# Optimization experiments

Hardware: AMD Instinct MI355X
Metric: run time of the kernel (lower is better)

Reference implementation:

```python
import jax, jax.numpy as jnp
import numpy as np

N, E = 50000, 800000
DIM_IN, DIM_OUT, HEADS, HID = 1000, 32, 8, 8
NEG_SLOPE = 0.2


def glorot(key, shape, fan_in, fan_out):
    s = jnp.sqrt(6.0 / (fan_in + fan_out))
    return jax.random.uniform(key, shape, jnp.float32, -s, s)


def setup_inputs() -> dict:
    key = jax.random.key(0)
    ks = jax.random.split(key, 16)
    x = jax.random.normal(ks[0], (N, DIM_IN), jnp.float32)
    edge_index = jax.random.randint(ks[1], (2, E), 0, N, jnp.int32)
    d2 = DIM_IN + HEADS * HID  # 1064
    p = {
        "x": x, "edge_index": edge_index,
        "W1": glorot(ks[2], (DIM_IN, HEADS * HID), DIM_IN, HEADS * HID),
        "as1": glorot(ks[3], (HEADS, HID), HID, HID),
        "ad1": glorot(ks[4], (HEADS, HID), HID, HID),
        "b1": jnp.zeros((HEADS * HID,), jnp.float32),
        "W2": glorot(ks[5], (d2, HEADS * HID), d2, HEADS * HID),
        "as2": glorot(ks[6], (HEADS, HID), HID, HID),
        "ad2": glorot(ks[7], (HEADS, HID), HID, HID),
        "b2": jnp.zeros((HEADS * HID,), jnp.float32),
        "W3": glorot(ks[8], (HEADS * HID, HEADS * DIM_OUT), HEADS * HID, HEADS * DIM_OUT),
        "as3": glorot(ks[9], (HEADS, DIM_OUT), DIM_OUT, DIM_OUT),
        "ad3": glorot(ks[10], (HEADS, DIM_OUT), DIM_OUT, DIM_OUT),
        "b3": jnp.zeros((DIM_OUT,), jnp.float32),
    }
    return p


def gat_conv(x, src, dst, W, a_src, a_dst, bias, heads, out_ch, concat):
    n = x.shape[0]
    h = (x @ W).reshape(n, heads, out_ch)           # [N,H,C]
    al_s = jnp.einsum("nhc,hc->nh", h, a_src)        # [N,H]
    al_d = jnp.einsum("nhc,hc->nh", h, a_dst)
    e = jax.nn.leaky_relu(al_s[src] + al_d[dst], NEG_SLOPE)  # [Etot,H]
    # segment softmax over incoming edges of each dst node
    m = jax.ops.segment_max(e, dst, num_segments=n)
    ee = jnp.exp(e - m[dst])
    denom = jax.ops.segment_sum(ee, dst, num_segments=n)
    alpha = ee / (denom[dst] + 1e-16)               # [Etot,H]
    msg = h[src] * alpha[..., None]                  # [Etot,H,C]
    out = jax.ops.segment_sum(msg, dst, num_segments=n)  # [N,H,C]
    out = out.reshape(n, heads * out_ch) if concat else out.mean(axis=1)
    return out + bias


def reference(x, edge_index, W1, as1, ad1, b1, W2, as2, ad2, b2, W3, as3, ad3, b3):
    n = x.shape[0]
    loops = jnp.arange(n, dtype=edge_index.dtype)
    src = jnp.concatenate([edge_index[0], loops])    # PyG adds self-loops
    dst = jnp.concatenate([edge_index[1], loops])
    h1 = jax.nn.elu(gat_conv(x, src, dst, W1, as1, ad1, b1, HEADS, HID, True))
    h2 = gat_conv(jnp.concatenate([x, h1], axis=1), src, dst, W2, as2, ad2, b2, HEADS, HID, True)
    h2 = jax.nn.elu(h2)
    h3 = gat_conv(h2, src, dst, W3, as3, ad3, b3, HEADS, DIM_OUT, False)
    return jax.nn.log_softmax(h3, axis=1)
```

## Files before the change

kernel.cpp:

```cpp
#include <hip/hip_runtime.h>
#include <hip/hip_bf16.h>

#define DIM_IN 1000
#define HEADS 8
#define HID 8
#define DIM_OUT 32
#define NEG_SLOPE 0.2f
#define EPAD 64

typedef __attribute__((ext_vector_type(4))) float f32x4;
typedef __attribute__((ext_vector_type(8))) short s16x8;

__device__ __forceinline__ unsigned bf16rne(float f) {
    unsigned u = __float_as_uint(f);
    return (u + 0x7FFFu + ((u >> 16) & 1u)) >> 16;
}
__device__ __forceinline__ unsigned pack2(float lo, float hi) {
    return bf16rne(lo) | (bf16rne(hi) << 16);
}
__device__ __forceinline__ float bflo(unsigned u) { return __uint_as_float(u << 16); }
__device__ __forceinline__ float bfhi(unsigned u) { return __uint_as_float(u & 0xFFFF0000u); }
__device__ __forceinline__ float bf1(ushort u) { return __uint_as_float((unsigned)u << 16); }

__global__ __launch_bounds__(256) void pack_all(
    const float* __restrict__ W1, const float* __restrict__ W2,
    const float* __restrict__ W3, const float* __restrict__ as3,
    const float* __restrict__ ad3, ushort* __restrict__ wpack,
    ushort* __restrict__ w3pack, float* __restrict__ wts,
    float* __restrict__ wtd)
{
    int b = blockIdx.x;
    if (b < 64) {
        int t = b * 256 + threadIdx.x;
        int lane = t & 63;
        int ctg = (t >> 6) & 7;
        int kt = t >> 9;
        int c = ctg * 16 + (lane & 15);
        int kbase = kt * 32 + (lane >> 4) * 8;
        ushort v[8] __attribute__((aligned(16)));
#pragma unroll
        for (int j = 0; j < 8; j++) {
            int k = kbase + j;
            float w = 0.f;
            if (k < DIM_IN) w = (c < 64) ? W1[(size_t)k * 64 + c] : W2[(size_t)k * 64 + (c - 64)];
            v[j] = (ushort)bf16rne(w);
        }
        *(uint4*)&wpack[(size_t)t * 8] = *(const uint4*)v;
    } else if (b < 72) {
        int t = (b - 64) * 256 + threadIdx.x;
        int lane = t & 63;
        int ctg = (t >> 6) & 15;
        int kt = t >> 10;
        int c = ctg * 16 + (lane & 15);
        int kbase = kt * 32 + (lane >> 4) * 8;
        ushort v[8] __attribute__((aligned(16)));
#pragma unroll
        for (int j = 0; j < 8; j++)
            v[j] = (ushort)bf16rne(W3[(size_t)(kbase + j) * 256 + c]);
        *(uint4*)&w3pack[(size_t)t * 8] = *(const uint4*)v;
    } else {
        int t = (b - 72) * 256 + threadIdx.x;
        if (t >= 512) return;
        int h = t >> 6, k = t & 63;
        float s = 0.f, d = 0.f;
#pragma unroll
        for (int c = 0; c < 32; c++) {
            float w = W3[(size_t)k * 256 + h * 32 + c];
            s += w * as3[h * 32 + c];
            d += w * ad3[h * 32 + c];
        }
        wts[h * 64 + k] = s;
        wtd[h * 64 + k] = d;
    }
}

__global__ __launch_bounds__(256) void zero_init(
    int* __restrict__ deg, int* __restrict__ esrc_pad, int N)
{
    int i = blockIdx.x * 256 + threadIdx.x;
    if (i < N) deg[i] = 0;
    if (i < EPAD) esrc_pad[i] = 0;
}

__global__ __launch_bounds__(256) void gemm1_mfma(
    const float* __restrict__ x, const ushort* __restrict__ wpack,
    ushort* __restrict__ hp1b, float* __restrict__ p2, int N)
{
    __shared__ __align__(16) ushort a_lds[2][32 * 32];
    const int tid = threadIdx.x;
    const int lane = tid & 63;
    const int wc = tid >> 6;
    const int rowbase = blockIdx.x * 32;

    const int srow = tid >> 3;
    const int skq = (tid & 7) * 4;
    const int sgr = rowbase + srow;
    const int sidx = ((srow >> 4) * 64 + (skq >> 3) * 16 + (srow & 15)) * 8 + (skq & 4);

    f32x4 acc[2][2];
#pragma unroll
    for (int i = 0; i < 2; i++)
#pragma unroll
        for (int j = 0; j < 2; j++) acc[i][j] = (f32x4){0.f, 0.f, 0.f, 0.f};

    float4 s0;
    auto load_stage = [&](int t) {
        int k0 = t * 32 + skq;
        s0 = make_float4(0.f, 0.f, 0.f, 0.f);
        if (sgr < N && k0 + 4 <= DIM_IN)
            s0 = *(const float4*)&x[(size_t)sgr * DIM_IN + k0];
    };
    auto store_stage = [&](int buf) {
        uint2 w;
        w.x = pack2(s0.x, s0.y);
        w.y = pack2(s0.z, s0.w);
        *(uint2*)&a_lds[buf][sidx] = w;
    };

    load_stage(0);
    store_stage(0);
    __syncthreads();

    const s16x8* wp = (const s16x8*)wpack;
    for (int t = 0; t < 32; t++) {
        int cur = t & 1;
        if (t + 1 < 32) load_stage(t + 1);
        s16x8 bf0 = wp[(size_t)(t * 8 + wc * 2 + 0) * 64 + lane];
        s16x8 bf1 = wp[(size_t)(t * 8 + wc * 2 + 1) * 64 + lane];
        s16x8 af0 = *(const s16x8*)&a_lds[cur][(0 * 64 + lane) * 8];
        s16x8 af1 = *(const s16x8*)&a_lds[cur][(1 * 64 + lane) * 8];
        acc[0][0] = __builtin_amdgcn_mfma_f32_16x16x32_bf16(af0, bf0, acc[0][0], 0, 0, 0);
        acc[0][1] = __builtin_amdgcn_mfma_f32_16x16x32_bf16(af0, bf1, acc[0][1], 0, 0, 0);
        acc[1][0] = __builtin_amdgcn_mfma_f32_16x16x32_bf16(af1, bf0, acc[1][0], 0, 0, 0);
        acc[1][1] = __builtin_amdgcn_mfma_f32_16x16x32_bf16(af1, bf1, acc[1][1], 0, 0, 0);
        if (t + 1 < 32) store_stage(cur ^ 1);
        __syncthreads();
    }

    const int colbase = wc * 32;
#pragma unroll
    for (int rt = 0; rt < 2; rt++) {
        int gr = rowbase + rt * 16 + ((lane >> 4) * 4);
#pragma unroll
        for (int ctl = 0; ctl < 2; ctl++) {
            int c = colbase + ctl * 16 + (lane & 15);
#pragma unroll
            for (int reg = 0; reg < 4; reg++) {
                int r = gr + reg;
                if (r >= N) continue;
                float v = acc[rt][ctl][reg];
                if (c < 64) hp1b[(size_t)r * 64 + c] = (ushort)bf16rne(v);
                else        p2[(size_t)r * 64 + (c - 64)] = v;
            }
        }
    }
}

__global__ __launch_bounds__(256) void gemm3_mfma(
    const ushort* __restrict__ h2b, const ushort* __restrict__ w3pack,
    ushort* __restrict__ h3pb, int N)
{
    const int tid = threadIdx.x;
    const int lane = tid & 63;
    const int wc = tid >> 6;
    const int rowbase = blockIdx.x * 16;
    const int arow = rowbase + (lane & 15);

    f32x4 acc[4];
#pragma unroll
    for (int i = 0; i < 4; i++) acc[i] = (f32x4){0.f, 0.f, 0.f, 0.f};

    const s16x8* wp = (const s16x8*)w3pack;
#pragma unroll
    for (int kt = 0; kt < 2; kt++) {
        s16x8 af = (s16x8){0, 0, 0, 0, 0, 0, 0, 0};
        if (arow < N)
            af = *(const s16x8*)&h2b[(size_t)arow * 64 + kt * 32 + (lane >> 4) * 8];
#pragma unroll
        for (int ct = 0; ct < 4; ct++) {
            s16x8 bf = wp[(size_t)(kt * 16 + wc * 4 + ct) * 64 + lane];
            acc[ct] = __builtin_amdgcn_mfma_f32_16x16x32_bf16(af, bf, acc[ct], 0, 0, 0);
        }
    }
#pragma unroll
    for (int ct = 0; ct < 4; ct++) {
        int col = wc * 64 + ct * 16 + (lane & 15);
        int gr = rowbase + (lane >> 4) * 4;
#pragma unroll
        for (int reg = 0; reg < 4; reg++) {
            int r = gr + reg;
            if (r < N) h3pb[(size_t)r * 256 + col] = (ushort)bf16rne(acc[ct][reg]);
        }
    }
}

__global__ __launch_bounds__(256) void gemm_k64_n64_acc(
    const float* __restrict__ A, const float* __restrict__ W,
    const float* __restrict__ P, ushort* __restrict__ outb, int N)
{
    __shared__ float as_[16][65];
    const int tid = threadIdx.x;
    const int rb = blockIdx.x * 16;
#pragma unroll
    for (int i = 0; i < 4; i++) {
        int idx = tid + i * 256;
        int r = idx >> 6, c = idx & 63;
        int gr = rb + r;
        as_[r][c] = (gr < N) ? A[(size_t)gr * 64 + c] : 0.f;
    }
    __syncthreads();
    const int row = tid >> 4;
    const int col = (tid & 15) * 4;
    float4 acc = {0, 0, 0, 0};
#pragma unroll 8
    for (int k = 0; k < 64; k++) {
        float a = as_[row][k];
        float4 w = *(const float4*)&W[k * 64 + col];
        acc.x += a * w.x; acc.y += a * w.y; acc.z += a * w.z; acc.w += a * w.w;
    }
    int gr = rb + row;
    if (gr < N) {
        float4 p = *(const float4*)&P[(size_t)gr * 64 + col];
        float v0 = p.x + acc.x, v1 = p.y + acc.y, v2 = p.z + acc.z, v3 = p.w + acc.w;
        *(uint*)&outb[(size_t)gr * 64 + col] = pack2(v0, v1);
        *(uint*)&outb[(size_t)gr * 64 + col + 2] = pack2(v2, v3);
    }
}

__global__ __launch_bounds__(256) void attn_dots_b8(
    const ushort* __restrict__ hb, const float* __restrict__ a_s,
    const float* __restrict__ a_d, float* __restrict__ als,
    float* __restrict__ ald, int NH)
{
    int i = blockIdx.x * blockDim.x + threadIdx.x;
    if (i >= NH) return;
    int head = i & 7;
    uint4 q = *(const uint4*)&hb[(size_t)i * 8];
    float f[8] = {bflo(q.x), bfhi(q.x), bflo(q.y), bfhi(q.y),
                  bflo(q.z), bfhi(q.z), bflo(q.w), bfhi(q.w)};
    const float* ap = a_s + head * 8;
    const float* dp = a_d + head * 8;
    float s = 0.f, d = 0.f;
#pragma unroll
    for (int c = 0; c < 8; c++) { s += f[c] * ap[c]; d += f[c] * dp[c]; }
    als[i] = s; ald[i] = d;
}

__global__ __launch_bounds__(256) void attn_dots_w(
    const ushort* __restrict__ h2b, const float* __restrict__ wts,
    const float* __restrict__ wtd, float* __restrict__ als,
    float* __restrict__ ald, int NH)
{
    int i = blockIdx.x * blockDim.x + threadIdx.x;
    if (i >= NH) return;
    int head = i & 7, node = i >> 3;
    const uint4* hp = (const uint4*)(h2b + (size_t)node * 64);
    const float* wsp = wts + head * 64;
    const float* wdp = wtd + head * 64;
    float s = 0.f, d = 0.f;
#pragma unroll
    for (int cq = 0; cq < 8; cq++) {
        uint4 q = hp[cq];
        float f0 = bflo(q.x), f1 = bfhi(q.x), f2 = bflo(q.y), f3 = bfhi(q.y);
        float f4 = bflo(q.z), f5 = bfhi(q.z), f6 = bflo(q.w), f7 = bfhi(q.w);
        int c = cq * 8;
        s += f0 * wsp[c] + f1 * wsp[c + 1] + f2 * wsp[c + 2] + f3 * wsp[c + 3]
           + f4 * wsp[c + 4] + f5 * wsp[c + 5] + f6 * wsp[c + 6] + f7 * wsp[c + 7];
        d += f0 * wdp[c] + f1 * wdp[c + 1] + f2 * wdp[c + 2] + f3 * wdp[c + 3]
           + f4 * wdp[c + 4] + f5 * wdp[c + 5] + f6 * wdp[c + 6] + f7 * wdp[c + 7];
    }
    als[i] = s; ald[i] = d;
}

__global__ __launch_bounds__(256) void csr_hist(
    const int* __restrict__ ei, int E, int Etot, int* __restrict__ deg)
{
    int e = blockIdx.x * blockDim.x + threadIdx.x;
    if (e >= Etot) return;
    int d = (e < E) ? ei[E + e] : e - E;
    atomicAdd(&deg[d], 1);
}

__global__ __launch_bounds__(256) void scan_partial(
    const int* __restrict__ deg, int* __restrict__ bsum, int N)
{
    __shared__ int red[256];
    int base = blockIdx.x * 1024;
    int t = threadIdx.x;
    int i0 = base + t * 4;
    int s = 0;
    if (i0 + 3 < N) {
        int4 v = *(const int4*)&deg[i0];
        s = v.x + v.y + v.z + v.w;
    } else {
#pragma unroll
        for (int j = 0; j < 4; j++) if (i0 + j < N) s += deg[i0 + j];
    }
    red[t] = s;
    __syncthreads();
    for (int off = 128; off; off >>= 1) {
        if (t < off) red[t] += red[t + off];
        __syncthreads();
    }
    if (t == 0) bsum[blockIdx.x] = red[0];
}

__global__ __launch_bounds__(64) void scan_bsums(
    const int* __restrict__ bsum, int* __restrict__ boff,
    int* __restrict__ rowptr, int nb, int N)
{
    __shared__ int sh[256];
    int t = threadIdx.x;
    for (int i = t; i < nb; i += 64) sh[i] = bsum[i];
    __syncthreads();
    if (t == 0) {
        int run = 0;
        for (int i = 0; i < nb; i++) { int x = sh[i]; sh[i] = run; run += x; }
        rowptr[N] = run;
    }
    __syncthreads();
    for (int i = t; i < nb; i += 64) boff[i] = sh[i];
}

__global__ __launch_bounds__(256) void scan_final(
    const int* __restrict__ deg, const int* __restrict__ boff,
    int* __restrict__ rowptr, int* __restrict__ cursor, int N)
{
    __shared__ int red[256];
    int base = blockIdx.x * 1024;
    int t = threadIdx.x;
    int i0 = base + t * 4;
    int v0 = 0, v1 = 0, v2 = 0, v3 = 0;
    if (i0 + 3 < N) {
        int4 v = *(const int4*)&deg[i0];
        v0 = v.x; v1 = v.y; v2 = v.z; v3 = v.w;
    } else {
        if (i0 < N) v0 = deg[i0];
        if (i0 + 1 < N) v1 = deg[i0 + 1];
        if (i0 + 2 < N) v2 = deg[i0 + 2];
        if (i0 + 3 < N) v3 = deg[i0 + 3];
    }
    red[t] = v0 + v1 + v2 + v3;
    __syncthreads();
    for (int off = 1; off < 256; off <<= 1) {
        int n = (t >= off) ? red[t - off] : 0;
        __syncthreads();
        red[t] += n;
        __syncthreads();
    }
    int excl = (t ? red[t - 1] : 0) + boff[blockIdx.x];
    if (i0 < N)     { rowptr[i0] = excl;     cursor[i0] = excl; }
    excl += v0;
    if (i0 + 1 < N) { rowptr[i0 + 1] = excl; cursor[i0 + 1] = excl; }
    excl += v1;
    if (i0 + 2 < N) { rowptr[i0 + 2] = excl; cursor[i0 + 2] = excl; }
    excl += v2;
    if (i0 + 3 < N) { rowptr[i0 + 3] = excl; cursor[i0 + 3] = excl; }
}

__global__ __launch_bounds__(256) void csr_fill(
    const int* __restrict__ ei, int E, int Etot,
    int* __restrict__ cursor, int* __restrict__ esrc)
{
    int e = blockIdx.x * blockDim.x + threadIdx.x;
    if (e >= Etot) return;
    int s, d;
    if (e < E) { s = ei[e]; d = ei[E + e]; } else { s = d = e - E; }
    int pos = atomicAdd(&cursor[d], 1);
    esrc[pos] = s;
}

template <bool OUT_BF16>
__global__ __launch_bounds__(256) void gat_gather64(
    const int* __restrict__ rowptr, const int* __restrict__ esrc,
    const float* __restrict__ als, const float* __restrict__ ald,
    const ushort* __restrict__ hb, const float* __restrict__ bias,
    float* __restrict__ outf, ushort* __restrict__ outb, int N)
{
    int node = blockIdx.x * 4 + (threadIdx.x >> 6);
    if (node >= N) return;
    int lane = threadIdx.x & 63;
    int head = lane >> 3;
    int start = rowptr[node];
    int cnt = rowptr[node + 1] - start;
    float aldv = ald[(size_t)node * 8 + head];
    const int* ip = esrc + start;

    float dA = 0.f, aA = 0.f;
    float dB = 0.f, aB = 0.f;

    auto idx4 = [&](int k) {
        int4 r; r.x = ip[k]; r.y = ip[k + 1]; r.z = ip[k + 2]; r.w = ip[k + 3];
        return r;
    };
    auto issue = [&](int4 s, float4& ee, float4& hh) {
        ee.x = als[(size_t)s.x * 8 + head];
        ee.y = als[(size_t)s.y * 8 + head];
        ee.z = als[(size_t)s.z * 8 + head];
        ee.w = als[(size_t)s.w * 8 + head];
        hh.x = bf1(hb[(size_t)s.x * 64 + lane]);
        hh.y = bf1(hb[(size_t)s.y * 64 + lane]);
        hh.z = bf1(hb[(size_t)s.z * 64 + lane]);
        hh.w = bf1(hb[(size_t)s.w * 64 + lane]);
    };
    auto lrelu = [&](float e, int k) {
        e += aldv;
        e = (e > 0.f) ? e : NEG_SLOPE * e;
        return (k < cnt) ? e : -1e30f;
    };
    auto upd = [&](int base, float4 ee, float4 hh) {
        if (base >= cnt) return;
        float x0 = __expf(lrelu(ee.x, base + 0));
        float x1 = __expf(lrelu(ee.y, base + 1));
        float x2 = __expf(lrelu(ee.z, base + 2));
        float x3 = __expf(lrelu(ee.w, base + 3));
        dA += x0; aA = fmaf(x0, hh.x, aA);
        dA += x1; aA = fmaf(x1, hh.y, aA);
        dB += x2; aB = fmaf(x2, hh.z, aB);
        dB += x3; aB = fmaf(x3, hh.w, aB);
    };

    int4 i0 = idx4(0), i1 = idx4(4);
    float4 e0, h0, e1, h1;
    issue(i0, e0, h0);
    int nb = (cnt + 3) >> 2;
    for (int b = 0; b < nb; b += 2) {
        i0 = idx4((b + 2) * 4);
        issue(i1, e1, h1);
        upd(b * 4, e0, h0);
        i1 = idx4((b + 3) * 4);
        issue(i0, e0, h0);
        upd((b + 1) * 4, e1, h1);
    }
    float den = dA + dB;
    float acc = aA + aB;
    float v = acc / (den + 1e-16f) + bias[lane];
    v = (v > 0.f) ? v : (__expf(v) - 1.f);
    if (OUT_BF16) outb[(size_t)node * 64 + lane] = (ushort)bf16rne(v);
    else outf[(size_t)node * 64 + lane] = v;
}

__global__ __launch_bounds__(256) void gat_l3_final(
    const int* __restrict__ rowptr, const int* __restrict__ esrc,
    const float* __restrict__ als, const float* __restrict__ ald,
    const ushort* __restrict__ h3pb, const float* __restrict__ b3,
    float* __restrict__ out, int N)
{
    int node = blockIdx.x * 4 + (threadIdx.x >> 6);
    if (node >= N) return;
    int lane = threadIdx.x & 63;
    int h = lane >> 3, c8 = lane & 7;
    int loff = h * 32 + c8 * 4;
    int start = rowptr[node];
    int cnt = rowptr[node + 1] - start;
    float aldv = ald[(size_t)node * 8 + h];
    const int* ip = esrc + start;

    float dA = 0.f, dB = 0.f;
    float4 accA = {0, 0, 0, 0}, accB = {0, 0, 0, 0};

    auto idx4 = [&](int k) {
        int4 r; r.x = ip[k]; r.y = ip[k + 1]; r.z = ip[k + 2]; r.w = ip[k + 3];
        return r;
    };
    auto issue = [&](int4 s, float4& ee, uint2& q0, uint2& q1, uint2& q2, uint2& q3) {
        ee.x = als[(size_t)s.x * 8 + h];
        ee.y = als[(size_t)s.y * 8 + h];
        ee.z = als[(size_t)s.z * 8 + h];
        ee.w = als[(size_t)s.w * 8 + h];
        q0 = *(const uint2*)&h3pb[(size_t)s.x * 256 + loff];
        q1 = *(const uint2*)&h3pb[(size_t)s.y * 256 + loff];
        q2 = *(const uint2*)&h3pb[(size_t)s.z * 256 + loff];
        q3 = *(const uint2*)&h3pb[(size_t)s.w * 256 + loff];
    };
    auto lrelu = [&](float e, int k) {
        e += aldv;
        e = (e > 0.f) ? e : NEG_SLOPE * e;
        return (k < cnt) ? e : -1e30f;
    };
    auto upedge = [&](float ee, uint2 q, float& d, float4& a) {
        d += ee;
        a.x = fmaf(ee, bflo(q.x), a.x);
        a.y = fmaf(ee, bfhi(q.x), a.y);
        a.z = fmaf(ee, bflo(q.y), a.z);
        a.w = fmaf(ee, bfhi(q.y), a.w);
    };
    auto upd = [&](int base, float4 ee, uint2 q0, uint2 q1, uint2 q2, uint2 q3) {
        if (base >= cnt) return;
        float x0 = __expf(lrelu(ee.x, base + 0));
        float x1 = __expf(lrelu(ee.y, base + 1));
        float x2 = __expf(lrelu(ee.z, base + 2));
        float x3 = __expf(lrelu(ee.w, base + 3));
        upedge(x0, q0, dA, accA);
        upedge(x1, q1, dA, accA);
        upedge(x2, q2, dB, accB);
        upedge(x3, q3, dB, accB);
    };

    int4 i0 = idx4(0), i1 = idx4(4);
    float4 eC, eD;
    uint2 q0C, q1C, q2C, q3C, q0D, q1D, q2D, q3D;
    issue(i0, eC, q0C, q1C, q2C, q3C);
    int nb = (cnt + 3) >> 2;
    for (int b = 0; b < nb; b += 2) {
        i0 = idx4((b + 2) * 4);
        issue(i1, eD, q0D, q1D, q2D, q3D);
        upd(b * 4, eC, q0C, q1C, q2C, q3C);
        i1 = idx4((b + 3) * 4);
        issue(i0, eC, q0C, q1C, q2C, q3C);
        upd((b + 1) * 4, eD, q0D, q1D, q2D, q3D);
    }

    float den = dA + dB;
    float inv = 1.f / (den + 1e-16f);
    float4 v;
    v.x = (accA.x + accB.x) * inv;
    v.y = (accA.y + accB.y) * inv;
    v.z = (accA.z + accB.z) * inv;
    v.w = (accA.w + accB.w) * inv;

#pragma unroll
    for (int o = 8; o < 64; o <<= 1) {
        v.x += __shfl_xor(v.x, o, 64);
        v.y += __shfl_xor(v.y, o, 64);
        v.z += __shfl_xor(v.z, o, 64);
        v.w += __shfl_xor(v.w, o, 64);
    }
    int cq = c8 * 4;
    v.x = v.x * 0.125f + b3[cq + 0];
    v.y = v.y * 0.125f + b3[cq + 1];
    v.z = v.z * 0.125f + b3[cq + 2];
    v.w = v.w * 0.125f + b3[cq + 3];
    float mx = fmaxf(fmaxf(v.x, v.y), fmaxf(v.z, v.w));
#pragma unroll
    for (int o = 1; o < 8; o <<= 1) mx = fmaxf(mx, __shfl_xor(mx, o, 64));
    float ex = __expf(v.x - mx) + __expf(v.y - mx) + __expf(v.z - mx) + __expf(v.w - mx);
#pragma unroll
    for (int o = 1; o < 8; o <<= 1) ex += __shfl_xor(ex, o, 64);
    float lse = mx + __logf(ex);
    if (lane < 8) {
        float4 r4 = {v.x - lse, v.y - lse, v.z - lse, v.w - lse};
        *(float4*)&out[(size_t)node * 32 + cq] = r4;
    }
}

extern "C" void kernel_launch(void* const* d_in, const int* in_sizes, int n_in,
                              void* d_out, int out_size, void* d_ws, size_t ws_size,
                              hipStream_t stream)
{
    const float* x   = (const float*)d_in[0];
    const int*   ei  = (const int*)  d_in[1];
    const float* W1  = (const float*)d_in[2];
    const float* as1 = (const float*)d_in[3];
    const float* ad1 = (const float*)d_in[4];
    const float* b1  = (const float*)d_in[5];
    const float* W2  = (const float*)d_in[6];
    const float* as2 = (const float*)d_in[7];
    const float* ad2 = (const float*)d_in[8];
    const float* b2  = (const float*)d_in[9];
    const float* W3  = (const float*)d_in[10];
    const float* as3 = (const float*)d_in[11];
    const float* ad3 = (const float*)d_in[12];
    const float* b3  = (const float*)d_in[13];
    float* out = (float*)d_out;

    const int N = in_sizes[0] / DIM_IN;
    const int E = in_sizes[1] / 2;
    const int Etot = E + N;

    float* ws = (float*)d_ws;
    size_t o = 0;
    float* p2  = ws + o; o += (size_t)N * 64;
    float* h1  = ws + o; o += (size_t)N * 64;
    ushort* hp1b  = (ushort*)(ws + o); o += (size_t)N * 32;
    ushort* h2pb  = (ushort*)(ws + o); o += (size_t)N * 32;
    ushort* h2b   = (ushort*)(ws + o); o += (size_t)N * 32;
    ushort* h3pb  = (ushort*)(ws + o); o += (size_t)N * 128;
    float* als = ws + o; o += (size_t)N * 8;
    float* ald = ws + o; o += (size_t)N * 8;
    float* wts = ws + o; o += 512;
    float* wtd = ws + o; o += 512;
    ushort* wpack  = (ushort*)(ws + o); o += 65536;
    ushort* w3pack = (ushort*)(ws + o); o += 8192;
    int* deg    = (int*)(ws + o); o += N;
    int* rowptr = (int*)(ws + o); o += N + 1;
    int* cursor = (int*)(ws + o); o += N;
    int* bsum   = (int*)(ws + o); o += 64;
    int* boff   = (int*)(ws + o); o += 64;
    int* esrc   = (int*)(ws + o); o += Etot + EPAD;
    if (o * 4 > ws_size) return;

    const int TB = 256;
    const int EG = (Etot + TB - 1) / TB;
    const int NB = (N + 1023) / 1024;

    pack_all<<<74, TB, 0, stream>>>(W1, W2, W3, as3, ad3, wpack, w3pack, wts, wtd);
    gemm1_mfma<<<(N + 31) / 32, TB, 0, stream>>>(x, wpack, hp1b, p2, N);

    zero_init<<<(N + TB - 1) / TB, TB, 0, stream>>>(deg, esrc + Etot, N);
    csr_hist<<<EG, TB, 0, stream>>>(ei, E, Etot, deg);
    scan_partial<<<NB, TB, 0, stream>>>(deg, bsum, N);
    scan_bsums<<<1, 64, 0, stream>>>(bsum, boff, rowptr, NB, N);
    scan_final<<<NB, TB, 0, stream>>>(deg, boff, rowptr, cursor, N);
    csr_fill<<<EG, TB, 0, stream>>>(ei, E, Etot, cursor, esrc);

    attn_dots_b8<<<(N * 8 + TB - 1) / TB, TB, 0, stream>>>(hp1b, as1, ad1, als, ald, N * 8);
    gat_gather64<false><<<(N + 3) / 4, TB, 0, stream>>>(rowptr, esrc, als, ald, hp1b, b1, h1, nullptr, N);

    gemm_k64_n64_acc<<<(N + 15) / 16, TB, 0, stream>>>(h1, W2 + (size_t)DIM_IN * 64, p2, h2pb, N);

    attn_dots_b8<<<(N * 8 + TB - 1) / TB, TB, 0, stream>>>(h2pb, as2, ad2, als, ald, N * 8);
    gat_gather64<true><<<(N + 3) / 4, TB, 0, stream>>>(rowptr, esrc, als, ald, h2pb, b2, nullptr, h2b, N);

    gemm3_mfma<<<(N + 15) / 16, TB, 0, stream>>>(h2b, w3pack, h3pb, N);
    attn_dots_w<<<(N * 8 + TB - 1) / TB, TB, 0, stream>>>(h2b, wts, wtd, als, ald, N * 8);
    gat_l3_final<<<(N + 3) / 4, TB, 0, stream>>>(rowptr, esrc, als, ald, h3pb, b3, out, N);
}
```

Baseline: 400.9 us.

## Sort nodes by degree for gather kernels and widen gemm1 loads to 8 floats

Adds a degree histogram, bin scan and counting-sort permutation so the three gather kernels process nodes grouped by in-degree. Nodes with similar edge counts then share a block, which is meant to reduce wave imbalance and tail latency. Separately, gemm1 now loads 8 floats per thread per stage and covers two K-steps per LDS buffer pair, which halves the number of barriers. The cost is three extra small kernels with atomics, an indirect perm lookup that makes output writes non-contiguous, and a larger LDS footprint.

Result: slower. 683.9 us (+70.6%).

```diff
diff --git a/kernel.cpp b/kernel.cpp
--- a/kernel.cpp
+++ b/kernel.cpp
@@ -75,27 +75,29 @@
 }
 
 __global__ __launch_bounds__(256) void zero_init(
-    int* __restrict__ deg, int* __restrict__ esrc_pad, int N)
+    int* __restrict__ deg, int* __restrict__ esrc_pad, int* __restrict__ bins, int N)
 {
     int i = blockIdx.x * 256 + threadIdx.x;
     if (i < N) deg[i] = 0;
     if (i < EPAD) esrc_pad[i] = 0;
+    if (i < 64) bins[i] = 0;
 }
 
 __global__ __launch_bounds__(256) void gemm1_mfma(
     const float* __restrict__ x, const ushort* __restrict__ wpack,
     ushort* __restrict__ hp1b, float* __restrict__ p2, int N)
 {
-    __shared__ __align__(16) ushort a_lds[2][32 * 32];
+    __shared__ __align__(16) ushort a_lds[4][32 * 32];
     const int tid = threadIdx.x;
     const int lane = tid & 63;
     const int wc = tid >> 6;
     const int rowbase = blockIdx.x * 32;
 
     const int srow = tid >> 3;
-    const int skq = (tid & 7) * 4;
+    const int sj = tid & 7;
     const int sgr = rowbase + srow;
-    const int sidx = ((srow >> 4) * 64 + (skq >> 3) * 16 + (srow & 15)) * 8 + (skq & 4);
+    const int shalf = sj >> 2;
+    const int sidx = ((srow >> 4) * 64 + (sj & 3) * 16 + (srow & 15)) * 8;
 
     f32x4 acc[2][2];
 #pragma unroll
@@ -103,37 +105,47 @@
 #pragma unroll
         for (int j = 0; j < 2; j++) acc[i][j] = (f32x4){0.f, 0.f, 0.f, 0.f};
 
-    float4 s0;
-    auto load_stage = [&](int t) {
-        int k0 = t * 32 + skq;
-        s0 = make_float4(0.f, 0.f, 0.f, 0.f);
-        if (sgr < N && k0 + 4 <= DIM_IN)
-            s0 = *(const float4*)&x[(size_t)sgr * DIM_IN + k0];
-    };
-    auto store_stage = [&](int buf) {
-        uint2 w;
-        w.x = pack2(s0.x, s0.y);
-        w.y = pack2(s0.z, s0.w);
-        *(uint2*)&a_lds[buf][sidx] = w;
-    };
-
-    load_stage(0);
-    store_stage(0);
+    float4 r0, r1;
+    auto load_pair = [&](int p) {
+        int k0 = p * 64 + sj * 8;
+        r0 = make_float4(0.f, 0.f, 0.f, 0.f);
+        r1 = make_float4(0.f, 0.f, 0.f, 0.f);
+        if (sgr < N && k0 + 8 <= DIM_IN) {
+            const float* pp = &x[(size_t)sgr * DIM_IN + k0];
+            r0 = *(const float4*)pp;
+            r1 = *(const float4*)(pp + 4);
+        }
+    };
+    auto store_pair = [&](int bufbase) {
+        uint4 w;
+        w.x = pack2(r0.x, r0.y);
+        w.y = pack2(r0.z, r0.w);
+        w.z = pack2(r1.x, r1.y);
+        w.w = pack2(r1.z, r1.w);
+        *(uint4*)&a_lds[bufbase + shalf][sidx] = w;
+    };
+
+    load_pair(0);
+    store_pair(0);
     __syncthreads();
 
     const s16x8* wp = (const s16x8*)wpack;
-    for (int t = 0; t < 32; t++) {
-        int cur = t & 1;
-        if (t + 1 < 32) load_stage(t + 1);
-        s16x8 bf0 = wp[(size_t)(t * 8 + wc * 2 + 0) * 64 + lane];
-        s16x8 bf1 = wp[(size_t)(t * 8 + wc * 2 + 1) * 64 + lane];
-        s16x8 af0 = *(const s16x8*)&a_lds[cur][(0 * 64 + lane) * 8];
-        s16x8 af1 = *(const s16x8*)&a_lds[cur][(1 * 64 + lane) * 8];
-        acc[0][0] = __builtin_amdgcn_mfma_f32_16x16x32_bf16(af0, bf0, acc[0][0], 0, 0, 0);
-        acc[0][1] = __builtin_amdgcn_mfma_f32_16x16x32_bf16(af0, bf1, acc[0][1], 0, 0, 0);
-        acc[1][0] = __builtin_amdgcn_mfma_f32_16x16x32_bf16(af1, bf0, acc[1][0], 0, 0, 0);
-        acc[1][1] = __builtin_amdgcn_mfma_f32_16x16x32_bf16(af1, bf1, acc[1][1], 0, 0, 0);
-        if (t + 1 < 32) store_stage(cur ^ 1);
+    for (int p = 0; p < 16; p++) {
+        int rb = (p & 1) * 2;
+        if (p + 1 < 16) load_pair(p + 1);
+#pragma unroll
+        for (int half = 0; half < 2; half++) {
+            int t = p * 2 + half;
+            s16x8 bf0 = wp[(size_t)(t * 8 + wc * 2 + 0) * 64 + lane];
+            s16x8 bf1 = wp[(size_t)(t * 8 + wc * 2 + 1) * 64 + lane];
+            s16x8 af0 = *(const s16x8*)&a_lds[rb + half][(0 * 64 + lane) * 8];
+            s16x8 af1 = *(const s16x8*)&a_lds[rb + half][(1 * 64 + lane) * 8];
+            acc[0][0] = __builtin_amdgcn_mfma_f32_16x16x32_bf16(af0, bf0, acc[0][0], 0, 0, 0);
+            acc[0][1] = __builtin_amdgcn_mfma_f32_16x16x32_bf16(af0, bf1, acc[0][1], 0, 0, 0);
+            acc[1][0] = __builtin_amdgcn_mfma_f32_16x16x32_bf16(af1, bf0, acc[1][0], 0, 0, 0);
+            acc[1][1] = __builtin_amdgcn_mfma_f32_16x16x32_bf16(af1, bf1, acc[1][1], 0, 0, 0);
+        }
+        if (p + 1 < 16) store_pair(((p + 1) & 1) * 2);
         __syncthreads();
     }
 
@@ -279,6 +291,37 @@
     if (e >= Etot) return;
     int d = (e < E) ? ei[E + e] : e - E;
     atomicAdd(&deg[d], 1);
+}
+
+__global__ __launch_bounds__(256) void hist_deg(
+    const int* __restrict__ deg, int* __restrict__ bins, int N)
+{
+    int i = blockIdx.x * 256 + threadIdx.x;
+    if (i >= N) return;
+    atomicAdd(&bins[min(deg[i], 63)], 1);
+}
+
+__global__ __launch_bounds__(64) void scan_bins(
+    const int* __restrict__ bins, int* __restrict__ bincur)
+{
+    __shared__ int off[64];
+    int t = threadIdx.x;
+    if (t == 0) {
+        int run = 0;
+        for (int i = 0; i < 64; i++) { int v = bins[i]; off[i] = run; run += v; }
+    }
+    __syncthreads();
+    bincur[t] = off[t];
+}
+
+__global__ __launch_bounds__(256) void fill_perm(
+    const int* __restrict__ deg, int* __restrict__ bincur,
+    int* __restrict__ perm, int N)
+{
+    int i = blockIdx.x * 256 + threadIdx.x;
+    if (i >= N) return;
+    int pos = atomicAdd(&bincur[min(deg[i], 63)], 1);
+    perm[pos] = i;
 }
 
 __global__ __launch_bounds__(256) void scan_partial(
@@ -372,13 +415,15 @@
 
 template <bool OUT_BF16>
 __global__ __launch_bounds__(256) void gat_gather64(
-    const int* __restrict__ rowptr, const int* __restrict__ esrc,
-    const float* __restrict__ als, const float* __restrict__ ald,
-    const ushort* __restrict__ hb, const float* __restrict__ bias,
-    float* __restrict__ outf, ushort* __restrict__ outb, int N)
-{
-    int node = blockIdx.x * 4 + (threadIdx.x >> 6);
-    if (node >= N) return;
+    const int* __restrict__ perm, const int* __restrict__ rowptr,
+    const int* __restrict__ esrc, const float* __restrict__ als,
+    const float* __restrict__ ald, const ushort* __restrict__ hb,
+    const float* __restrict__ bias, float* __restrict__ outf,
+    ushort* __restrict__ outb, int N)
+{
+    int idx = blockIdx.x * 4 + (threadIdx.x >> 6);
+    if (idx >= N) return;
+    int node = perm[idx];
     int lane = threadIdx.x & 63;
     int head = lane >> 3;
     int start = rowptr[node];
@@ -441,13 +486,14 @@
 }
 
 __global__ __launch_bounds__(256) void gat_l3_final(
-    const int* __restrict__ rowptr, const int* __restrict__ esrc,
-    const float* __restrict__ als, const float* __restrict__ ald,
-    const ushort* __restrict__ h3pb, const float* __restrict__ b3,
-    float* __restrict__ out, int N)
-{
-    int node = blockIdx.x * 4 + (threadIdx.x >> 6);
-    if (node >= N) return;
+    const int* __restrict__ perm, const int* __restrict__ rowptr,
+    const int* __restrict__ esrc, const float* __restrict__ als,
+    const float* __restrict__ ald, const ushort* __restrict__ h3pb,
+    const float* __restrict__ b3, float* __restrict__ out, int N)
+{
+    int idx = blockIdx.x * 4 + (threadIdx.x >> 6);
+    if (idx >= N) return;
+    int node = perm[idx];
     int lane = threadIdx.x & 63;
     int h = lane >> 3, c8 = lane & 7;
     int loff = h * 32 + c8 * 4;
@@ -587,32 +633,39 @@
     int* cursor = (int*)(ws + o); o += N;
     int* bsum   = (int*)(ws + o); o += 64;
     int* boff   = (int*)(ws + o); o += 64;
+    int* bins   = (int*)(ws + o); o += 64;
+    int* bincur = (int*)(ws + o); o += 64;
+    int* perm   = (int*)(ws + o); o += N;
     int* esrc   = (int*)(ws + o); o += Etot + EPAD;
     if (o * 4 > ws_size) return;
 
     const int TB = 256;
     const int EG = (Etot + TB - 1) / TB;
     const int NB = (N + 1023) / 1024;
+    const int NG = (N + TB - 1) / TB;
 
     pack_all<<<74, TB, 0, stream>>>(W1, W2, W3, as3, ad3, wpack, w3pack, wts, wtd);
     gemm1_mfma<<<(N + 31) / 32, TB, 0, stream>>>(x, wpack, hp1b, p2, N);
 
-    zero_init<<<(N + TB - 1) / TB, TB, 0, stream>>>(deg, esrc + Etot, N);
+    zero_init<<<NG, TB, 0, stream>>>(deg, esrc + Etot, bins, N);
     csr_hist<<<EG, TB, 0, stream>>>(ei, E, Etot, deg);
+    hist_deg<<<NG, TB, 0, stream>>>(deg, bins, N);
     scan_partial<<<NB, TB, 0, stream>>>(deg, bsum, N);
     scan_bsums<<<1, 64, 0, stream>>>(bsum, boff, rowptr, NB, N);
     scan_final<<<NB, TB, 0, stream>>>(deg, boff, rowptr, cursor, N);
+    scan_bins<<<1, 64, 0, stream>>>(bins, bincur);
+    fill_perm<<<NG, TB, 0, stream>>>(deg, bincur, perm, N);
     csr_fill<<<EG, TB, 0, stream>>>(ei, E, Etot, cursor, esrc);
 
     attn_dots_b8<<<(N * 8 + TB - 1) / TB, TB, 0, stream>>>(hp1b, as1, ad1, als, ald, N * 8);
-    gat_gather64<false><<<(N + 3) / 4, TB, 0, stream>>>(rowptr, esrc, als, ald, hp1b, b1, h1, nullptr, N);
+    gat_gather64<false><<<(N + 3) / 4, TB, 0, stream>>>(perm, rowptr, esrc, als, ald, hp1b, b1, h1, nullptr, N);
 
     gemm_k64_n64_acc<<<(N + 15) / 16, TB, 0, stream>>>(h1, W2 + (size_t)DIM_IN * 64, p2, h2pb, N);
 
     attn_dots_b8<<<(N * 8 + TB - 1) / TB, TB, 0, stream>>>(h2pb, as2, ad2, als, ald, N * 8);
-    gat_gather64<true><<<(N + 3) / 4, TB, 0, stream>>>(rowptr, esrc, als, ald, h2pb, b2, nullptr, h2b, N);
+    gat_gather64<true><<<(N + 3) / 4, TB, 0, stream>>>(perm, rowptr, esrc, als, ald, h2pb, b2, nullptr, h2b, N);
 
     gemm3_mfma<<<(N + 15) / 16, TB, 0, stream>>>(h2b, w3pack, h3pb, N);
     attn_dots_w<<<(N * 8 + TB - 1) / TB, TB, 0, stream>>>(h2b, wts, wtd, als, ald, N * 8);
-    gat_l3_final<<<(N + 3) / 4, TB, 0, stream>>>(rowptr, esrc, als, ald, h3pb, b3, out, N);
-}
+    gat_l3_final<<<(N + 3) / 4, TB, 0, stream>>>(perm, rowptr, esrc, als, ald, h3pb, b3, out, N);
+}
```
